# Performance work log

Hardware: AMD Instinct MI355X
Metric: run time of the kernel (lower is better)

Reference implementation:

```python
import jax, jax.numpy as jnp
import numpy as np

NR = 8192
M = 8192


def setup_inputs() -> dict:
    key = jax.random.key(0)
    k1, _ = jax.random.split(key)
    C = jax.random.normal(k1, (M, NR), dtype=jnp.float32)
    D = jnp.ones((NR,), dtype=jnp.float32)  # nn.Parameter(torch.ones(Nr))
    return {"C": C, "D": D}


def reference(C, D):
    # C @ diag(D) is exactly column-wise scaling of C by D.
    # Broadcasting multiply computes the same math without materializing
    # the [Nr, Nr] diagonal matrix or running a dense GEMM.
    return C * D[None, :]
```

## Files before the change

kernel.cpp:

```cpp
#include <hip/hip_runtime.h>
#include <hip/hip_bf16.h>


#define NR 8192
#define M_ROWS 8192

__global__ __launch_bounds__(256) void colscale_kernel(
    const float4* __restrict__ C4,
    const float4* __restrict__ D4,
    float4* __restrict__ O4)
{
    const unsigned i = blockIdx.x * blockDim.x + threadIdx.x;
    const float4 c = C4[i];
    const float4 d = D4[i & (NR / 4 - 1)];
    float4 o;
    o.x = c.x * d.x;
    o.y = c.y * d.y;
    o.z = c.z * d.z;
    o.w = c.w * d.w;
    O4[i] = o;
}

extern "C" void kernel_launch(void* const* d_in, const int* in_sizes, int n_in,
                              void* d_out, int out_size, void* d_ws, size_t ws_size,
                              hipStream_t stream) {
    const float4* C4 = (const float4*)d_in[0];
    const float4* D4 = (const float4*)d_in[1];
    float4* O4 = (float4*)d_out;

    const int n4 = (M_ROWS * NR) / 4;
    const int threads = 256;
    const int blocks = n4 / threads;

    colscale_kernel<<<blocks, threads, 0, stream>>>(C4, D4, O4);
}
```

Before: 417.1 us.

## Process 32 rows per thread with reused D and nontemporal loads/stores

```diff
diff --git a/kernel.cpp b/kernel.cpp
--- a/kernel.cpp
+++ b/kernel.cpp
@@ -2,35 +2,41 @@
 #include <hip/hip_bf16.h>
 
 
-#define NR 8192
+#define NR     8192
 #define M_ROWS 8192
+#define NR4    (NR / 4)
+#define ROWS_PT 32
+
+typedef float v4f __attribute__((ext_vector_type(4)));
 
 __global__ __launch_bounds__(256) void colscale_kernel(
-    const float4* __restrict__ C4,
-    const float4* __restrict__ D4,
-    float4* __restrict__ O4)
+    const v4f* __restrict__ C4,
+    const v4f* __restrict__ D4,
+    v4f* __restrict__ O4)
 {
-    const unsigned i = blockIdx.x * blockDim.x + threadIdx.x;
-    const float4 c = C4[i];
-    const float4 d = D4[i & (NR / 4 - 1)];
-    float4 o;
-    o.x = c.x * d.x;
-    o.y = c.y * d.y;
-    o.z = c.z * d.z;
-    o.w = c.w * d.w;
-    O4[i] = o;
+    const unsigned c4   = blockIdx.x * 256u + threadIdx.x;
+    const unsigned base = blockIdx.y * (ROWS_PT * NR4) + c4;
+
+    const v4f d = D4[c4];
+
+#pragma unroll 8
+    for (int r = 0; r < ROWS_PT; ++r) {
+        const unsigned idx = base + (unsigned)r * NR4;
+        v4f c = __builtin_nontemporal_load(&C4[idx]);
+        v4f o = c * d;
+        __builtin_nontemporal_store(o, &O4[idx]);
+    }
 }
 
 extern "C" void kernel_launch(void* const* d_in, const int* in_sizes, int n_in,
                               void* d_out, int out_size, void* d_ws, size_t ws_size,
                               hipStream_t stream) {
-    const float4* C4 = (const float4*)d_in[0];
-    const float4* D4 = (const float4*)d_in[1];
-    float4* O4 = (float4*)d_out;
+    const v4f* C4 = (const v4f*)d_in[0];
+    const v4f* D4 = (const v4f*)d_in[1];
+    v4f* O4 = (v4f*)d_out;
 
-    const int n4 = (M_ROWS * NR) / 4;
-    const int threads = 256;
-    const int blocks = n4 / threads;
+    dim3 grid(NR4 / 256, M_ROWS / ROWS_PT);
+    dim3 block(256);
 
-    colscale_kernel<<<blocks, threads, 0, stream>>>(C4, D4, O4);
+    colscale_kernel<<<grid, block, 0, stream>>>(C4, D4, O4);
 }
```

Measured after the change: 427.7 us. 2.5% more time.
